# Kernel tuning notes

Hardware: AMD Instinct MI355X
Metric: run time of the kernel (lower is better)

## Reference

```python
import jax, jax.numpy as jnp
import numpy as np

EMBED_DIM = 1024
ATTN_DIM = 1024


def setup_inputs() -> dict:
    key = jax.random.key(0)
    k1, k2, k3, k4 = jax.random.split(key, 4)
    embedded = jax.random.normal(k1, (4, 2048, EMBED_DIM), dtype=jnp.float32)
    # torch nn.Linear weights are [out_features, in_features]
    s = 1.0 / np.sqrt(EMBED_DIM)
    Wk = jax.random.uniform(k2, (ATTN_DIM, EMBED_DIM), jnp.float32, -s, s)
    Wq = jax.random.uniform(k3, (ATTN_DIM, EMBED_DIM), jnp.float32, -s, s)
    Wv = jax.random.uniform(k4, (ATTN_DIM, EMBED_DIM), jnp.float32, -s, s)
    return {"embedded": embedded, "Wk": Wk, "Wq": Wq, "Wv": Wv}


def reference(embedded, Wk, Wq, Wv):
    # projections: x @ W.T  (torch Linear, no bias)
    k = jnp.einsum("bse,ae->bsa", embedded, Wk)
    q = jnp.einsum("bse,ae->bsa", embedded, Wq)
    v = jnp.einsum("bse,ae->bsa", embedded, Wv)
    scale = 1.0 / jnp.sqrt(jnp.float32(ATTN_DIM))
    attn = jnp.einsum("bqa,bka->bqk", q, k) * scale  # [B, S, S]
    S = attn.shape[1]
    causal = jnp.tril(jnp.ones((S, S), dtype=bool))
    attn = jnp.where(causal[None, :, :], attn, -jnp.inf)
    a = jax.nn.softmax(attn, axis=2)
    out = jnp.einsum("bqk,bka->bqa", a, v)
    return jnp.round(out, 4)
```

## Files before the change

kernel.cpp:

```cpp
#include <hip/hip_runtime.h>
#include <hip/hip_bf16.h>
#include <hip/hip_fp16.h>
#include <stdint.h>

typedef __bf16 bf16_t;
typedef bf16_t bf16x8 __attribute__((ext_vector_type(8)));
typedef bf16_t bf16x4 __attribute__((ext_vector_type(4)));
typedef float f32x4 __attribute__((ext_vector_type(4)));

#define BM 128
#define BN 128
#define BK 64

__device__ __forceinline__ void gload_lds16(const void* g, void* l) {
    __builtin_amdgcn_global_load_lds(
        (const __attribute__((address_space(1))) void*)(uintptr_t)g,
        (__attribute__((address_space(3))) void*)(uintptr_t)l,
        16, 0, 0);
}

template <int EPI>
__device__ __forceinline__ void gemm_body(
    bf16_t* __restrict__ As, bf16_t* __restrict__ Bs,
    const bf16_t* __restrict__ A, long lda,
    const bf16_t* __restrict__ B, long ldb,
    void* __restrict__ Cv, long ldc,
    int k0beg, int k1end, float scale, int m0, int n0,
    float* __restrict__ rs)
{
    const int tid = threadIdx.x;
    const int wid = tid >> 6, lane = tid & 63;
    const int wr = wid >> 1, wc = wid & 1;
    const int hw = lane >> 4, ln = lane & 15;

    const int row0 = tid >> 2;
    const int jj = ((tid & 3) - (tid >> 3)) & 3;
    const bf16_t* srcA0 = A + (size_t)(m0 + row0) * lda + jj * 8;
    const bf16_t* srcB0 = B + (size_t)(n0 + row0) * ldb + jj * 8;

    f32x4 acc[4][4] = {};

    for (int k0 = k0beg; k0 < k1end; k0 += BK) {
#pragma unroll
        for (int i = 0; i < 4; i++) {
            const size_t roff = (size_t)((i & 1) * 64);
            const int koff = k0 + (i >> 1) * 32;
            gload_lds16(srcA0 + roff * lda + koff, &As[i * 2048 + tid * 8]);
            gload_lds16(srcB0 + roff * ldb + koff, &Bs[i * 2048 + tid * 8]);
        }
        __syncthreads();

#pragma unroll
        for (int h = 0; h < 2; h++) {
            bf16x8 af[4], bfr[4];
#pragma unroll
            for (int t = 0; t < 4; t++) {
                const int r  = wr * 64 + t * 16 + ln;
                const int rb = wc * 64 + t * 16 + ln;
                af[t]  = *(const bf16x8*)&As[h * 4096 + r  * 32 + (((hw + (r  >> 1)) & 3) * 8)];
                bfr[t] = *(const bf16x8*)&Bs[h * 4096 + rb * 32 + (((hw + (rb >> 1)) & 3) * 8)];
            }
#pragma unroll
            for (int ti = 0; ti < 4; ti++)
#pragma unroll
                for (int tj = 0; tj < 4; tj++)
                    acc[ti][tj] = __builtin_amdgcn_mfma_f32_16x16x32_bf16(
                        af[ti], bfr[tj], acc[ti][tj], 0, 0, 0);
        }
        __syncthreads();
    }

#pragma unroll
    for (int ti = 0; ti < 4; ti++) {
        const int rbase = m0 + wr * 64 + ti * 16 + hw * 4;
        f32x4 inv4;
        if (EPI == 2) {
            const float4 r4 = *(const float4*)&rs[rbase];
            inv4[0] = 1.0f / r4.x; inv4[1] = 1.0f / r4.y;
            inv4[2] = 1.0f / r4.z; inv4[3] = 1.0f / r4.w;
        }
        float part[4] = {0.f, 0.f, 0.f, 0.f};
#pragma unroll
        for (int tj = 0; tj < 4; tj++) {
            const int col = n0 + wc * 64 + tj * 16 + ln;
            if (EPI == 4) {
                const int bb = rbase >> 11;
                const int s  = rbase & 2047;
                const int d  = col - 2048;
                bf16x4 o;
#pragma unroll
                for (int rg = 0; rg < 4; rg++) o[rg] = (bf16_t)acc[ti][tj][rg];
                *(bf16x4*)&((bf16_t*)Cv)[(size_t)bb * 2097152 + (size_t)d * 2048 + s] = o;
            } else {
#pragma unroll
                for (int rg = 0; rg < 4; rg++) {
                    const size_t idx = (size_t)(rbase + rg) * ldc + col;
                    if (EPI == 2) {
                        ((float*)Cv)[idx] = acc[ti][tj][rg] * inv4[rg];
                    } else {
                        const float e = (col <= rbase + rg)
                                      ? __expf(acc[ti][tj][rg] * scale) : 0.0f;
                        part[rg] += e;
                        ((bf16_t*)Cv)[idx] = (bf16_t)e;
                    }
                }
            }
        }
        if (EPI == 3) {
#pragma unroll
            for (int rg = 0; rg < 4; rg++) {
                float p = part[rg];
                p += __shfl_xor(p, 1, 64);
                p += __shfl_xor(p, 2, 64);
                p += __shfl_xor(p, 4, 64);
                p += __shfl_xor(p, 8, 64);
                if (ln == 0) atomicAdd(&rs[rbase + rg], p);
            }
        }
    }
}

__device__ __forceinline__ void gemm256_body(
    bf16_t* __restrict__ lds,
    const bf16_t* __restrict__ A, long lda,
    const bf16_t* __restrict__ B, long ldb,
    bf16_t* __restrict__ C, long ldc,
    int nt, int m0, int n0)
{
    const int tid = threadIdx.x;
    const int wid = tid >> 6, lane = tid & 63;
    const int wr = wid >> 2, wcn = wid & 3;
    const int hw = lane >> 4, ln = lane & 15;

    const int srow = (wid << 3) + (lane >> 3);
    const int clog = ((lane & 7) - (lane >> 3)) & 7;
    const bf16_t* sA = A + (size_t)(m0 + srow) * lda + clog * 8;
    const bf16_t* sB = B + (size_t)(n0 + srow) * ldb + clog * 8;
    char* ldsc = (char*)lds;
    const int wb = wid << 10;

#define STG_A(bf, q, kt) gload_lds16(sA + (size_t)(q) * 64 * lda + (size_t)(kt) * 64, \
                                     ldsc + (bf) * 65536 + (q) * 8192 + wb)
#define STG_B(bf, q, kt) gload_lds16(sB + (size_t)(q) * 64 * ldb + (size_t)(kt) * 64, \
                                     ldsc + (bf) * 65536 + 32768 + (q) * 8192 + wb)

    const int c0 = ((hw + ln) & 7) << 4;
    const int c1 = ((hw + ln + 4) & 7) << 4;
    const int aR = (wr * 128 + ln) * 128;
    const int bR = 32768 + (wcn * 64 + ln) * 128;

#define RDA(bf, fr, ks) (*(const bf16x8*)(ldsc + (bf) * 65536 + aR + (fr) * 2048 + ((ks) ? c1 : c0)))
#define RDB(bf, fc, ks) (*(const bf16x8*)(ldsc + (bf) * 65536 + bR + (fc) * 2048 + ((ks) ? c1 : c0)))

    f32x4 acc[8][4] = {};

    STG_A(0, 0, 0); STG_A(0, 2, 0); STG_B(0, 0, 0); STG_B(0, 1, 0);
    STG_A(0, 1, 0); STG_A(0, 3, 0); STG_B(0, 2, 0); STG_B(0, 3, 0);
    STG_A(1, 0, 1); STG_A(1, 2, 1); STG_B(1, 0, 1); STG_B(1, 1, 1);
    STG_A(1, 1, 1); STG_A(1, 3, 1);
    asm volatile("s_waitcnt vmcnt(6)" ::: "memory");
    __builtin_amdgcn_s_barrier();

    for (int t = 0; t < nt; ++t) {
        const int bc = t & 1, bn = bc ^ 1;
        const int kt1 = (t + 1) & (nt - 1);
        const int kt2 = (t + 2) & (nt - 1);
        bf16x8 af[4][2], bl[2][2], bh[2][2];

#pragma unroll
        for (int fr = 0; fr < 4; ++fr) {
            af[fr][0] = RDA(bc, fr, 0);
            af[fr][1] = RDA(bc, fr, 1);
        }
#pragma unroll
        for (int fc = 0; fc < 2; ++fc) {
            bl[fc][0] = RDB(bc, fc, 0);
            bl[fc][1] = RDB(bc, fc, 1);
        }
        STG_B(bn, 2, kt1); STG_B(bn, 3, kt1);
        __builtin_amdgcn_s_barrier();
        asm volatile("s_waitcnt lgkmcnt(0)" ::: "memory");
        __builtin_amdgcn_sched_barrier(0);
        __builtin_amdgcn_s_setprio(1);
#pragma unroll
        for (int fr = 0; fr < 4; ++fr)
#pragma unroll
            for (int fc = 0; fc < 2; ++fc)
#pragma unroll
                for (int ks = 0; ks < 2; ++ks)
                    acc[fr][fc] = __builtin_amdgcn_mfma_f32_16x16x32_bf16(
                        af[fr][ks], bl[fc][ks], acc[fr][fc], 0, 0, 0);
        __builtin_amdgcn_s_setprio(0);
        __builtin_amdgcn_s_barrier();

#pragma unroll
        for (int fc = 0; fc < 2; ++fc) {
            bh[fc][0] = RDB(bc, fc + 2, 0);
            bh[fc][1] = RDB(bc, fc + 2, 1);
        }
        STG_A(bc, 0, kt2); STG_A(bc, 2, kt2);
        __builtin_amdgcn_s_barrier();
        asm volatile("s_waitcnt lgkmcnt(0)" ::: "memory");
        __builtin_amdgcn_sched_barrier(0);
        __builtin_amdgcn_s_setprio(1);
#pragma unroll
        for (int fr = 0; fr < 4; ++fr)
#pragma unroll
            for (int fc = 0; fc < 2; ++fc)
#pragma unroll
                for (int ks = 0; ks < 2; ++ks)
                    acc[fr][fc + 2] = __builtin_amdgcn_mfma_f32_16x16x32_bf16(
                        af[fr][ks], bh[fc][ks], acc[fr][fc + 2], 0, 0, 0);
        __builtin_amdgcn_s_setprio(0);
        __builtin_amdgcn_s_barrier();

#pragma unroll
        for (int fr = 0; fr < 4; ++fr) {
            af[fr][0] = RDA(bc, fr + 4, 0);
            af[fr][1] = RDA(bc, fr + 4, 1);
        }
        STG_B(bc, 0, kt2); STG_B(bc, 1, kt2);
        __builtin_amdgcn_s_barrier();
        asm volatile("s_waitcnt lgkmcnt(0)" ::: "memory");
        __builtin_amdgcn_sched_barrier(0);
        __builtin_amdgcn_s_setprio(1);
#pragma unroll
        for (int fr = 0; fr < 4; ++fr)
#pragma unroll
            for (int fc = 0; fc < 2; ++fc)
#pragma unroll
                for (int ks = 0; ks < 2; ++ks)
                    acc[fr + 4][fc + 2] = __builtin_amdgcn_mfma_f32_16x16x32_bf16(
                        af[fr][ks], bh[fc][ks], acc[fr + 4][fc + 2], 0, 0, 0);
        __builtin_amdgcn_s_setprio(0);
        __builtin_amdgcn_s_barrier();

        STG_A(bc, 1, kt2); STG_A(bc, 3, kt2);
        __builtin_amdgcn_s_setprio(1);
#pragma unroll
        for (int fr = 0; fr < 4; ++fr)
#pragma unroll
            for (int fc = 0; fc < 2; ++fc)
#pragma unroll
                for (int ks = 0; ks < 2; ++ks)
                    acc[fr + 4][fc] = __builtin_amdgcn_mfma_f32_16x16x32_bf16(
                        af[fr][ks], bl[fc][ks], acc[fr + 4][fc], 0, 0, 0);
        __builtin_amdgcn_s_setprio(0);
        asm volatile("s_waitcnt vmcnt(6)" ::: "memory");
        __builtin_amdgcn_s_barrier();
    }

    asm volatile("s_waitcnt vmcnt(0)" ::: "memory");

#pragma unroll
    for (int fr = 0; fr < 8; ++fr) {
        const int rbase = m0 + wr * 128 + fr * 16 + hw * 4;
#pragma unroll
        for (int fc = 0; fc < 4; ++fc) {
            const int col = n0 + wcn * 64 + fc * 16 + ln;
#pragma unroll
            for (int rg = 0; rg < 4; rg++)
                C[(size_t)(rbase + rg) * ldc + col] = (bf16_t)acc[fr][fc][rg];
        }
    }
#undef STG_A
#undef STG_B
#undef RDA
#undef RDB
}

__device__ __forceinline__ void qk_tile(int q, int& b, int& my, int& nx) {
    b = q & 3;
    int rem = q >> 2;
    my = 15; nx = 0;
#pragma unroll
    for (int m = 15; m >= 0; --m) {
        if (rem < m + 1) { my = m; nx = rem; break; }
        rem -= m + 1;
    }
}

__global__ __launch_bounds__(256) void cast_all(
    const float* __restrict__ x,
    const float* __restrict__ Wk, const float* __restrict__ Wq,
    const float* __restrict__ Wv,
    bf16_t* __restrict__ xb, bf16_t* __restrict__ Wb,
    float* __restrict__ rowsum)
{
    for (int u = blockIdx.x; u < 11272; u += gridDim.x) {
        if (u >= 11264) {
            const size_t i = ((size_t)(u - 11264) * 256 + threadIdx.x) * 4;
            *(float4*)(rowsum + i) = make_float4(0.f, 0.f, 0.f, 0.f);
            continue;
        }
        const float* src;
        bf16_t* dst;
        if (u < 8192) {
            const size_t i = ((size_t)u * 256 + threadIdx.x) * 4;
            src = x + i;
            dst = xb + i;
        } else {
            const size_t j = ((size_t)(u - 8192) * 256 + threadIdx.x) * 4;
            dst = Wb + j;
            if (j < (size_t)1048576)      src = Wk + j;
            else if (j < (size_t)2097152) src = Wq + (j - 1048576);
            else                          src = Wv + (j - 2097152);
        }
        const float4 v = *(const float4*)src;
        bf16x4 o;
        o.x = (bf16_t)v.x; o.y = (bf16_t)v.y; o.z = (bf16_t)v.z; o.w = (bf16_t)v.w;
        *(bf16x4*)dst = o;
    }
}

__global__ __launch_bounds__(512, 2) void gemm1_kq(
    const bf16_t* __restrict__ xb, const bf16_t* __restrict__ Wb,
    bf16_t* __restrict__ QKVb)
{
    __shared__ __align__(16) bf16_t lds[65536];
    const int lin = blockIdx.x;
    const int xcd = lin & 7;
    const int j   = lin >> 3;
    const int mblk = xcd * 4 + (j & 3);
    const int nblk = j >> 2;
    gemm256_body(lds, xb, 1024, Wb, 1024, QKVb, 2048, 16, mblk * 256, nblk * 256);
}

__global__ __launch_bounds__(256) void vqk_fused(
    const bf16_t* __restrict__ xb, const bf16_t* __restrict__ Wb,
    bf16_t* __restrict__ Vt,
    const bf16_t* __restrict__ QKVb, bf16_t* __restrict__ E,
    float* __restrict__ rowsum)
{
    __shared__ __align__(16) bf16_t As[BM * BK];
    __shared__ __align__(16) bf16_t Bs[BN * BK];
    const int id = blockIdx.x;
    if (id < 512) {
        const int xcd = id & 7;
        const int j   = id >> 3;
        const int mblk = xcd * 8 + (j >> 3);
        const int nblk = j & 7;
        gemm_body<4>(As, Bs, xb, 1024, Wb, 1024, Vt, 2048,
                     0, 1024, 1.0f, mblk * BM, 2048 + nblk * BN, nullptr);
    } else {
        int b, my, nx;
        qk_tile(id - 512, b, my, nx);
        const bf16_t* base = QKVb + (size_t)b * (2048L * 2048);
        gemm_body<3>(As, Bs,
                     base + 1024, 2048,
                     base, 2048,
                     E + (size_t)b * (2048L * 2048), 2048,
                     0, 1024, 0.03125f, my * BM, nx * BN,
                     rowsum + b * 2048);
    }
}

__global__ __launch_bounds__(256) void gemm1_v(
    const bf16_t* __restrict__ xb, const bf16_t* __restrict__ Wb,
    bf16_t* __restrict__ Vt)
{
    __shared__ __align__(16) bf16_t As[BM * BK];
    __shared__ __align__(16) bf16_t Bs[BN * BK];
    const int lin = blockIdx.x;
    const int xcd = lin & 7;
    const int j   = lin >> 3;
    const int mblk = xcd * 8 + (j >> 3);
    const int nblk = j & 7;
    gemm_body<4>(As, Bs, xb, 1024, Wb, 1024, Vt, 2048,
                 0, 1024, 1.0f, mblk * BM, 2048 + nblk * BN, nullptr);
}

__global__ __launch_bounds__(256) void qk_gemm(
    const bf16_t* __restrict__ QKVb, bf16_t* __restrict__ E,
    float* __restrict__ rowsum)
{
    __shared__ __align__(16) bf16_t As[BM * BK];
    __shared__ __align__(16) bf16_t Bs[BN * BK];
    int b, my, nx;
    qk_tile(blockIdx.x, b, my, nx);
    const bf16_t* base = QKVb + (size_t)b * (2048L * 2048);
    gemm_body<3>(As, Bs,
                 base + 1024, 2048,
                 base, 2048,
                 E + (size_t)b * (2048L * 2048), 2048,
                 0, 1024, 0.03125f, my * BM, nx * BN,
                 rowsum + b * 2048);
}

__global__ __launch_bounds__(256) void gemm3_pv(
    const bf16_t* __restrict__ E, const bf16_t* __restrict__ Vt,
    const float* __restrict__ rowsum, float* __restrict__ out)
{
    __shared__ __align__(16) bf16_t As[BM * BK];
    __shared__ __align__(16) bf16_t Bs[BN * BK];
    const int id = blockIdx.x;
    const int strip = (id < 256) ? (15 - (id >> 5)) : ((id - 256) >> 5);
    const int nx = (id >> 2) & 7;
    const int b = id & 3;
    const int m0 = strip * BM;
    gemm_body<2>(As, Bs,
                 E + (size_t)b * (2048L * 2048), 2048,
                 Vt + (size_t)b * (1024L * 2048), 2048,
                 out + (size_t)b * (2048L * 1024), 1024,
                 0, m0 + BM, 1.0f, m0, nx * BN,
                 (float*)rowsum + b * 2048);
}

extern "C" void kernel_launch(void* const* d_in, const int* in_sizes, int n_in,
                              void* d_out, int out_size, void* d_ws, size_t ws_size,
                              hipStream_t stream)
{
    const float* x  = (const float*)d_in[0];
    const float* Wk = (const float*)d_in[1];
    const float* Wq = (const float*)d_in[2];
    const float* Wv = (const float*)d_in[3];
    char* ws = (char*)d_ws;

    bf16_t* QKVb = (bf16_t*)(ws);
    bf16_t* Vt   = (bf16_t*)(ws + ((size_t)32 << 20));
    bf16_t* xb   = (bf16_t*)(ws + ((size_t)48 << 20));
    bf16_t* Wb   = (bf16_t*)(ws + ((size_t)64 << 20));
    const bool big = ws_size >= ((size_t)107 << 20);
    bf16_t* E      = (bf16_t*)(ws + ((size_t)(big ? 72 : 48) << 20));
    float*  rowsum = (float*)(ws + ((size_t)(big ? 106 : 80) << 20));
    float*  out    = (float*)d_out;

    cast_all<<<2048, 256, 0, stream>>>(x, Wk, Wq, Wv, xb, Wb, rowsum);

    gemm1_kq<<<256, 512, 0, stream>>>(xb, Wb, QKVb);

    if (big) {
        vqk_fused<<<1056, 256, 0, stream>>>(xb, Wb, Vt, QKVb, E, rowsum);
    } else {
        gemm1_v<<<512, 256, 0, stream>>>(xb, Wb, Vt);
        qk_gemm<<<544, 256, 0, stream>>>(QKVb, E, rowsum);
    }

    gemm3_pv<<<512, 256, 0, stream>>>(E, Vt, rowsum, out);
}
```

Baseline: 221.4 us.

## Reorder GEMM main loop to split phases by K-half and reschedule tile loads

The inner loop of the bf16 MFMA GEMM is regrouped into four phases. Each phase now covers one K-half and one M-half across all four N fragments, where before each phase covered both K-halves over half of N. This shrinks the live fragment registers from 16 to 8 bf16x8 vectors. The global-to-LDS staging is redistributed: the next tile's A and B halves are issued together early, and the k+2 loads are grouped in the last phase, with the vmcnt waits adjusted to match. The goal is lower register pressure and better overlap of loads with MFMA. The risk is more LDS fragment reads per iteration, plus subtle hazards in buffer reuse ordering.

```diff
diff --git a/kernel.cpp b/kernel.cpp
--- a/kernel.cpp
+++ b/kernel.cpp
@@ -154,29 +154,23 @@
 
     f32x4 acc[8][4] = {};
 
-    STG_A(0, 0, 0); STG_A(0, 2, 0); STG_B(0, 0, 0); STG_B(0, 1, 0);
-    STG_A(0, 1, 0); STG_A(0, 3, 0); STG_B(0, 2, 0); STG_B(0, 3, 0);
+    STG_A(0, 0, 0); STG_A(0, 1, 0); STG_A(0, 2, 0); STG_A(0, 3, 0);
+    STG_B(0, 0, 0); STG_B(0, 1, 0); STG_B(0, 2, 0); STG_B(0, 3, 0);
     STG_A(1, 0, 1); STG_A(1, 2, 1); STG_B(1, 0, 1); STG_B(1, 1, 1);
-    STG_A(1, 1, 1); STG_A(1, 3, 1);
-    asm volatile("s_waitcnt vmcnt(6)" ::: "memory");
+    asm volatile("s_waitcnt vmcnt(4)" ::: "memory");
     __builtin_amdgcn_s_barrier();
 
     for (int t = 0; t < nt; ++t) {
         const int bc = t & 1, bn = bc ^ 1;
         const int kt1 = (t + 1) & (nt - 1);
         const int kt2 = (t + 2) & (nt - 1);
-        bf16x8 af[4][2], bl[2][2], bh[2][2];
-
-#pragma unroll
-        for (int fr = 0; fr < 4; ++fr) {
-            af[fr][0] = RDA(bc, fr, 0);
-            af[fr][1] = RDA(bc, fr, 1);
-        }
-#pragma unroll
-        for (int fc = 0; fc < 2; ++fc) {
-            bl[fc][0] = RDB(bc, fc, 0);
-            bl[fc][1] = RDB(bc, fc, 1);
-        }
+        bf16x8 a[4], b[4];
+
+#pragma unroll
+        for (int fr = 0; fr < 4; ++fr) a[fr] = RDA(bc, fr, 0);
+#pragma unroll
+        for (int fc = 0; fc < 4; ++fc) b[fc] = RDB(bc, fc, 0);
+        STG_A(bn, 1, kt1); STG_A(bn, 3, kt1);
         STG_B(bn, 2, kt1); STG_B(bn, 3, kt1);
         __builtin_amdgcn_s_barrier();
         asm volatile("s_waitcnt lgkmcnt(0)" ::: "memory");
@@ -185,20 +179,14 @@
 #pragma unroll
         for (int fr = 0; fr < 4; ++fr)
 #pragma unroll
-            for (int fc = 0; fc < 2; ++fc)
-#pragma unroll
-                for (int ks = 0; ks < 2; ++ks)
-                    acc[fr][fc] = __builtin_amdgcn_mfma_f32_16x16x32_bf16(
-                        af[fr][ks], bl[fc][ks], acc[fr][fc], 0, 0, 0);
+            for (int fc = 0; fc < 4; ++fc)
+                acc[fr][fc] = __builtin_amdgcn_mfma_f32_16x16x32_bf16(
+                    a[fr], b[fc], acc[fr][fc], 0, 0, 0);
         __builtin_amdgcn_s_setprio(0);
         __builtin_amdgcn_s_barrier();
 
 #pragma unroll
-        for (int fc = 0; fc < 2; ++fc) {
-            bh[fc][0] = RDB(bc, fc + 2, 0);
-            bh[fc][1] = RDB(bc, fc + 2, 1);
-        }
-        STG_A(bc, 0, kt2); STG_A(bc, 2, kt2);
+        for (int fr = 0; fr < 4; ++fr) a[fr] = RDA(bc, fr + 4, 0);
         __builtin_amdgcn_s_barrier();
         asm volatile("s_waitcnt lgkmcnt(0)" ::: "memory");
         __builtin_amdgcn_sched_barrier(0);
@@ -206,20 +194,16 @@
 #pragma unroll
         for (int fr = 0; fr < 4; ++fr)
 #pragma unroll
-            for (int fc = 0; fc < 2; ++fc)
-#pragma unroll
-                for (int ks = 0; ks < 2; ++ks)
-                    acc[fr][fc + 2] = __builtin_amdgcn_mfma_f32_16x16x32_bf16(
-                        af[fr][ks], bh[fc][ks], acc[fr][fc + 2], 0, 0, 0);
+            for (int fc = 0; fc < 4; ++fc)
+                acc[fr + 4][fc] = __builtin_amdgcn_mfma_f32_16x16x32_bf16(
+                    a[fr], b[fc], acc[fr + 4][fc], 0, 0, 0);
         __builtin_amdgcn_s_setprio(0);
         __builtin_amdgcn_s_barrier();
 
 #pragma unroll
-        for (int fr = 0; fr < 4; ++fr) {
-            af[fr][0] = RDA(bc, fr + 4, 0);
-            af[fr][1] = RDA(bc, fr + 4, 1);
-        }
-        STG_B(bc, 0, kt2); STG_B(bc, 1, kt2);
+        for (int fr = 0; fr < 4; ++fr) a[fr] = RDA(bc, fr, 1);
+#pragma unroll
+        for (int fc = 0; fc < 4; ++fc) b[fc] = RDB(bc, fc, 1);
         __builtin_amdgcn_s_barrier();
         asm volatile("s_waitcnt lgkmcnt(0)" ::: "memory");
         __builtin_amdgcn_sched_barrier(0);
@@ -227,26 +211,28 @@
 #pragma unroll
         for (int fr = 0; fr < 4; ++fr)
 #pragma unroll
-            for (int fc = 0; fc < 2; ++fc)
-#pragma unroll
-                for (int ks = 0; ks < 2; ++ks)
-                    acc[fr + 4][fc + 2] = __builtin_amdgcn_mfma_f32_16x16x32_bf16(
-                        af[fr][ks], bh[fc][ks], acc[fr + 4][fc + 2], 0, 0, 0);
+            for (int fc = 0; fc < 4; ++fc)
+                acc[fr][fc] = __builtin_amdgcn_mfma_f32_16x16x32_bf16(
+                    a[fr], b[fc], acc[fr][fc], 0, 0, 0);
         __builtin_amdgcn_s_setprio(0);
         __builtin_amdgcn_s_barrier();
 
-        STG_A(bc, 1, kt2); STG_A(bc, 3, kt2);
+#pragma unroll
+        for (int fr = 0; fr < 4; ++fr) a[fr] = RDA(bc, fr + 4, 1);
+        STG_A(bc, 0, kt2); STG_A(bc, 2, kt2);
+        STG_B(bc, 0, kt2); STG_B(bc, 1, kt2);
+        __builtin_amdgcn_s_barrier();
+        asm volatile("s_waitcnt lgkmcnt(0)" ::: "memory");
+        __builtin_amdgcn_sched_barrier(0);
         __builtin_amdgcn_s_setprio(1);
 #pragma unroll
         for (int fr = 0; fr < 4; ++fr)
 #pragma unroll
-            for (int fc = 0; fc < 2; ++fc)
-#pragma unroll
-                for (int ks = 0; ks < 2; ++ks)
-                    acc[fr + 4][fc] = __builtin_amdgcn_mfma_f32_16x16x32_bf16(
-                        af[fr][ks], bl[fc][ks], acc[fr + 4][fc], 0, 0, 0);
+            for (int fc = 0; fc < 4; ++fc)
+                acc[fr + 4][fc] = __builtin_amdgcn_mfma_f32_16x16x32_bf16(
+                    a[fr], b[fc], acc[fr + 4][fc], 0, 0, 0);
         __builtin_amdgcn_s_setprio(0);
-        asm volatile("s_waitcnt vmcnt(6)" ::: "memory");
+        asm volatile("s_waitcnt vmcnt(4)" ::: "memory");
         __builtin_amdgcn_s_barrier();
     }
 
```

Result: no change. 222.3 us (+0.4%).
